# Optimization experiments

Hardware: AMD Instinct MI355X
Metric: run time of the kernel (lower is better)

Reference implementation:

```python
import jax, jax.numpy as jnp
import numpy as np

D_MODEL = 1024
NUM_HEADS = 16
HEAD_DIM = D_MODEL // NUM_HEADS
WINDOW = 64
BATCH = 2
SEQ = 2048


def setup_inputs() -> dict:
    key = jax.random.key(0)
    ks = jax.random.split(key, 5)
    s = 1.0 / np.sqrt(D_MODEL)  # torch Linear-ish init scale
    x = jax.random.normal(ks[0], (BATCH, SEQ, D_MODEL), dtype=jnp.float32)
    Wq = jax.random.normal(ks[1], (D_MODEL, D_MODEL), dtype=jnp.float32) * s
    Wk = jax.random.normal(ks[2], (D_MODEL, D_MODEL), dtype=jnp.float32) * s
    Wv = jax.random.normal(ks[3], (D_MODEL, D_MODEL), dtype=jnp.float32) * s
    Wo = jax.random.normal(ks[4], (D_MODEL, D_MODEL), dtype=jnp.float32) * s
    z = jnp.zeros((D_MODEL,), dtype=jnp.float32)
    return {"x": x, "Wq": Wq, "bq": z, "Wk": Wk, "bk": z, "Wv": Wv, "bv": z,
            "Wo": Wo, "bo": z}


def reference(x, Wq, bq, Wk, bk, Wv, bv, Wo, bo):
    B, S, D = x.shape
    H, Hd = NUM_HEADS, HEAD_DIM
    # QKV projections; weights stored as [in, out] so y = x @ W + b
    q = (x @ Wq + bq).reshape(B, S, H, Hd).transpose(0, 2, 1, 3)  # bhsd
    k = (x @ Wk + bk).reshape(B, S, H, Hd).transpose(0, 2, 1, 3)
    v = (x @ Wv + bv).reshape(B, S, H, Hd).transpose(0, 2, 1, 3)
    scores = jnp.einsum('bhqd,bhkd->bhqk', q, k) / jnp.sqrt(jnp.float32(Hd))
    # static local-window band mask: attend only where |i - j| <= window_size
    idx = jnp.arange(S)
    dist = jnp.abs(idx[None, :] - idx[:, None])  # [S, S]
    scores = jnp.where(dist[None, None] > WINDOW, -jnp.inf, scores)
    attn = jax.nn.softmax(scores, axis=-1)
    out = jnp.einsum('bhqk,bhkd->bhqd', attn, v)
    out = out.transpose(0, 2, 1, 3).reshape(B, S, D)
    return out @ Wo + bo
```

## Files before the change

kernel.cpp:

```cpp
#include <hip/hip_runtime.h>
#include <cstdint>
#include <cstddef>

typedef __bf16 bf16x8 __attribute__((ext_vector_type(8)));
typedef float  f32x4  __attribute__((ext_vector_type(4)));

__device__ __forceinline__ unsigned short f2bf(float f) {
    union { __bf16 b; unsigned short u; } cv; cv.b = (__bf16)f; return cv.u;
}
__device__ __forceinline__ int iclamp(int v, int lo, int hi) {
    return v < lo ? lo : (v > hi ? hi : v);
}

__device__ __forceinline__ void gload16(const void* gsrc, void* ldsdst) {
    __builtin_amdgcn_global_load_lds(
        (const __attribute__((address_space(1))) unsigned int*)(uintptr_t)gsrc,
        (__attribute__((address_space(3))) unsigned int*)(uintptr_t)ldsdst,
        16, 0, 0);
}

#define MFMA16(a, b, c) __builtin_amdgcn_mfma_f32_16x16x32_bf16((a), (b), (c), 0, 0, 0)

__global__ __launch_bounds__(256) void prep_k(const float* __restrict__ x,
                                              const float* __restrict__ Wq,
                                              const float* __restrict__ Wk,
                                              const float* __restrict__ Wv,
                                              const float* __restrict__ Wo,
                                              const float* __restrict__ bq,
                                              const float* __restrict__ bk,
                                              const float* __restrict__ bv,
                                              unsigned short* __restrict__ xb,
                                              unsigned short* __restrict__ Wt,
                                              float* __restrict__ bc) {
    __shared__ float tile[64][65];
    const int bx = blockIdx.x, tid = threadIdx.x;
    if (bx < 1024) {
        const int z = bx >> 8, t = bx & 255;
        const float* W = (z == 0) ? Wq : (z == 1) ? Wk : (z == 2) ? Wv : Wo;
        const int n0 = (t & 15) * 64, k0 = (t >> 4) * 64;
        const int tr = tid >> 4, tc = (tid & 15) * 4;
#pragma unroll
        for (int i = 0; i < 4; ++i) {
            int r = tr + i * 16;
            float4 v = *(const float4*)(W + (size_t)(k0 + r) * 1024 + n0 + tc);
            tile[r][tc + 0] = v.x; tile[r][tc + 1] = v.y;
            tile[r][tc + 2] = v.z; tile[r][tc + 3] = v.w;
        }
        __syncthreads();
        const int n = tid & 63, kc = (tid >> 6) * 16;
        union { unsigned short u[16]; uint4 q[2]; } pk;
#pragma unroll
        for (int c = 0; c < 16; ++c) pk.u[c] = f2bf(tile[kc + c][n]);
        uint4* dst = (uint4*)(Wt + (size_t)z * 1048576 + (size_t)(n0 + n) * 1024 + k0 + kc);
        dst[0] = pk.q[0]; dst[1] = pk.q[1];
    } else if (bx < 3072) {
        size_t i = ((size_t)(bx - 1024) * 256 + tid) * 8;
        float4 a = *(const float4*)(x + i);
        float4 b = *(const float4*)(x + i + 4);
        union { unsigned short u[8]; uint4 q; } pk;
        pk.u[0] = f2bf(a.x); pk.u[1] = f2bf(a.y); pk.u[2] = f2bf(a.z); pk.u[3] = f2bf(a.w);
        pk.u[4] = f2bf(b.x); pk.u[5] = f2bf(b.y); pk.u[6] = f2bf(b.z); pk.u[7] = f2bf(b.w);
        *(uint4*)(xb + i) = pk.q;
    } else {
        int i = (bx - 3072) * 256 + tid;
        bc[i] = (i < 1024) ? bq[i] : (i < 2048) ? bk[i - 1024] : bv[i - 2048];
    }
}

__global__ __launch_bounds__(256, 3) void gemm_qkv(const unsigned short* __restrict__ xb,
                                                   const unsigned short* __restrict__ Wt,
                                                   const float* __restrict__ bcat,
                                                   unsigned short* __restrict__ Qb,
                                                   unsigned short* __restrict__ Kb,
                                                   unsigned short* __restrict__ Vt) {
    __shared__ __align__(16) unsigned short Asm[128 * 64];
    __shared__ __align__(16) unsigned short Bsm[128 * 64];
    const int tid = threadIdx.x, wave = tid >> 6, lane = tid & 63;
    const int lq = lane & 15, quad = lane >> 4;
    const int m0 = blockIdx.y * 128, n0 = blockIdx.x * 128;

    f32x4 acc[4][4];
#pragma unroll
    for (int i = 0; i < 4; ++i)
#pragma unroll
        for (int j = 0; j < 4; ++j) acc[i][j] = f32x4{0.f, 0.f, 0.f, 0.f};

    const int nloc = (wave & 1) * 64;
    float bi[4];
#pragma unroll
    for (int j = 0; j < 4; ++j) bi[j] = bcat[n0 + nloc + j * 16 + lq];

    const int r8 = lane >> 3, cs = lane & 7;
    const int gch = (cs ^ r8) * 8;
    const unsigned short* gA[4];
    const unsigned short* gB[4];
    unsigned short* lA[4];
    unsigned short* lB[4];
#pragma unroll
    for (int s = 0; s < 4; ++s) {
        const int r = wave * 32 + s * 8 + r8;
        gA[s] = xb + (size_t)(m0 + r) * 1024 + gch;
        gB[s] = Wt + (size_t)(n0 + r) * 1024 + gch;
        lA[s] = Asm + (wave * 32 + s * 8) * 64;
        lB[s] = Bsm + (wave * 32 + s * 8) * 64;
    }

    int offA[4][2], offB[4][2];
#pragma unroll
    for (int i = 0; i < 4; ++i)
#pragma unroll
        for (int kk = 0; kk < 2; ++kk) {
            const int rA = (wave >> 1) * 64 + i * 16 + lq;
            const int rB = (wave & 1) * 64 + i * 16 + lq;
            offA[i][kk] = rA * 64 + (((kk * 4 + quad) ^ (lq & 7)) * 8);
            offB[i][kk] = rB * 64 + (((kk * 4 + quad) ^ (lq & 7)) * 8);
        }

    for (int kt = 0; kt < 1024; kt += 64) {
#pragma unroll
        for (int s = 0; s < 4; ++s) gload16(gA[s] + kt, lA[s]);
#pragma unroll
        for (int s = 0; s < 4; ++s) gload16(gB[s] + kt, lB[s]);
        __syncthreads();
#pragma unroll
        for (int kk = 0; kk < 2; ++kk) {
            bf16x8 af[4], bfr[4];
#pragma unroll
            for (int i = 0; i < 4; ++i) af[i] = *(const bf16x8*)(Asm + offA[i][kk]);
#pragma unroll
            for (int j = 0; j < 4; ++j) bfr[j] = *(const bf16x8*)(Bsm + offB[j][kk]);
#pragma unroll
            for (int i = 0; i < 4; ++i)
#pragma unroll
                for (int j = 0; j < 4; ++j)
                    acc[i][j] = MFMA16(af[i], bfr[j], acc[i][j]);
        }
        __syncthreads();
    }

    const int p = n0 >> 10;
    const int c64 = (n0 + nloc) & 1023;
    const int h = c64 >> 6;
    const int b = m0 >> 11;
    const int mw = m0 + (wave >> 1) * 64;
    const int mloc = mw & 2047;
    unsigned short* sw = Asm + wave * 1152;

    unsigned short* qkbase = (p == 0) ? Qb : Kb;

#pragma unroll
    for (int i = 0; i < 4; ++i) {
#pragma unroll
        for (int j = 0; j < 4; ++j)
#pragma unroll
            for (int r = 0; r < 4; ++r)
                sw[(quad * 4 + r) * 72 + j * 16 + lq] = f2bf(acc[i][j][r] + bi[j]);
        if (p < 2) {
            const int row = lane >> 2, c0 = (lane & 3) * 8;
            uint4 v0 = *(const uint4*)(sw + row * 72 + c0);
            uint4 v1 = *(const uint4*)(sw + row * 72 + c0 + 32);
            const int s = mloc + i * 16 + row;
            unsigned short* dp = qkbase + ((size_t)((b * 16 + h) * 2048 + s)) * 64;
            *(uint4*)(dp + c0) = v0;
            *(uint4*)(dp + c0 + 32) = v1;
        } else {
#pragma unroll
            for (int th = 0; th < 2; ++th) {
                union { unsigned short u[8]; uint4 q; } pk;
#pragma unroll
                for (int t = 0; t < 8; ++t) pk.u[t] = sw[(th * 8 + t) * 72 + lane];
                const int sbase = mloc + i * 16 + th * 8;
                *(uint4*)(Vt + ((size_t)((b * 16 + h) * 64 + lane)) * 2048 + sbase) = pk.q;
            }
        }
    }
}

__global__ __launch_bounds__(256, 4) void attn_k(const unsigned short* __restrict__ Qb,
                                                 const unsigned short* __restrict__ Kb,
                                                 const unsigned short* __restrict__ Vt,
                                                 unsigned short* __restrict__ AO) {
    __shared__ __align__(16) unsigned short P[4][16 * 168];
    const int tid = threadIdx.x, wave = tid >> 6, lane = tid & 63;
    const int lq = lane & 15, quad = lane >> 4;
    const int b = blockIdx.z, h = blockIdx.y;
    const int q0 = blockIdx.x * 64 + wave * 16;
    const bool edge = (blockIdx.x == 0) || (blockIdx.x == 31);
    const unsigned short* Qh = Qb + (size_t)((b * 16 + h) * 2048) * 64;
    const unsigned short* Kh = Kb + (size_t)((b * 16 + h) * 2048) * 64;
    const unsigned short* Vh = Vt + (size_t)((b * 16 + h) * 64) * 2048;
    unsigned short* pw = P[wave];

    {
        unsigned int* zp = (unsigned int*)(pw + (lane >> 2) * 168 + 144 + (lane & 3) * 4);
        zp[0] = 0u; zp[1] = 0u;
    }

    const bf16x8 qa0 = *(const bf16x8*)(Qh + (size_t)(q0 + lq) * 64 + quad * 8);
    const bf16x8 qa1 = *(const bf16x8*)(Qh + (size_t)(q0 + lq) * 64 + 32 + quad * 8);

    float pr[9][4];
    float ls[4] = {0.f, 0.f, 0.f, 0.f};
#pragma unroll
    for (int t = 0; t < 9; ++t) {
        const int krow = q0 - 64 + t * 16 + lq;
        const bool need_mask = (t == 0) || (t == 8) || edge;
        const int krc = need_mask ? iclamp(krow, 0, 2047) : krow;
        const unsigned short* kp = Kh + (size_t)krc * 64 + quad * 8;
        const bf16x8 kf0 = *(const bf16x8*)kp;
        const bf16x8 kf1 = *(const bf16x8*)(kp + 32);
        f32x4 cacc = f32x4{0.f, 0.f, 0.f, 0.f};
        cacc = MFMA16(qa0, kf0, cacc);
        cacc = MFMA16(qa1, kf1, cacc);
        if (need_mask) {
#pragma unroll
            for (int r = 0; r < 4; ++r) {
                const int q = q0 + quad * 4 + r;
                const int dj = q - krow;
                const bool ok = (krow >= 0) && (krow < 2048) && (dj <= 64) && (dj >= -64);
                const float pv = ok ? __expf(cacc[r] * 0.125f) : 0.f;
                pr[t][r] = pv;
                ls[r] += pv;
            }
        } else {
#pragma unroll
            for (int r = 0; r < 4; ++r) {
                const float pv = __expf(cacc[r] * 0.125f);
                pr[t][r] = pv;
                ls[r] += pv;
            }
        }
    }
#pragma unroll
    for (int r = 0; r < 4; ++r) {
#pragma unroll
        for (int off = 1; off < 16; off <<= 1)
            ls[r] += __shfl_xor(ls[r], off);
    }
    float rinv[4];
#pragma unroll
    for (int r = 0; r < 4; ++r) rinv[r] = 1.f / ls[r];

#pragma unroll
    for (int t = 0; t < 9; ++t)
#pragma unroll
        for (int r = 0; r < 4; ++r)
            pw[(quad * 4 + r) * 168 + t * 16 + lq] = f2bf(pr[t][r]);

    f32x4 oa[4];
#pragma unroll
    for (int dt = 0; dt < 4; ++dt) oa[dt] = f32x4{0.f, 0.f, 0.f, 0.f};
#pragma unroll
    for (int ks = 0; ks < 5; ++ks) {
        const bf16x8 pf = *(const bf16x8*)(pw + lq * 168 + ks * 32 + quad * 8);
        int s0 = q0 - 64 + ks * 32 + quad * 8;
        s0 = iclamp(s0, 0, 2040);
#pragma unroll
        for (int dt = 0; dt < 4; ++dt) {
            const bf16x8 vf = *(const bf16x8*)(Vh + (size_t)(dt * 16 + lq) * 2048 + s0);
            oa[dt] = MFMA16(pf, vf, oa[dt]);
        }
    }

#pragma unroll
    for (int dt = 0; dt < 4; ++dt)
#pragma unroll
        for (int r = 0; r < 4; ++r)
            pw[(quad * 4 + r) * 72 + dt * 16 + lq] = f2bf(oa[dt][r] * rinv[r]);
    {
        const int row = lane >> 2, c0 = (lane & 3) * 16;
        uint4 v0 = *(const uint4*)(pw + row * 72 + c0);
        uint4 v1 = *(const uint4*)(pw + row * 72 + c0 + 8);
        unsigned short* dp = AO + (size_t)(b * 2048 + q0 + row) * 1024 + h * 64 + c0;
        *(uint4*)(dp) = v0;
        *(uint4*)(dp + 8) = v1;
    }
}

__global__ __launch_bounds__(256, 2) void gemm_out(const unsigned short* __restrict__ AO,
                                                   const unsigned short* __restrict__ Wot,
                                                   const float* __restrict__ bo,
                                                   float* __restrict__ out) {
    __shared__ __align__(16) unsigned short Asm[128 * 64];
    __shared__ __align__(16) unsigned short Bsm[64 * 64];
    const int tid = threadIdx.x, wave = tid >> 6, lane = tid & 63;
    const int lq = lane & 15, quad = lane >> 4;
    const int m0 = blockIdx.y * 128, n0 = blockIdx.x * 64;

    f32x4 acc[4][2];
#pragma unroll
    for (int i = 0; i < 4; ++i)
#pragma unroll
        for (int j = 0; j < 2; ++j) acc[i][j] = f32x4{0.f, 0.f, 0.f, 0.f};

    float bi[2];
#pragma unroll
    for (int j = 0; j < 2; ++j) bi[j] = bo[n0 + (wave & 1) * 32 + j * 16 + lq];

    const int r8 = lane >> 3, cs = lane & 7;
    const int gch = (cs ^ r8) * 8;
    const unsigned short* gA[4];
    unsigned short* lA[4];
#pragma unroll
    for (int s = 0; s < 4; ++s) {
        const int r = wave * 32 + s * 8 + r8;
        gA[s] = AO + (size_t)(m0 + r) * 1024 + gch;
        lA[s] = Asm + (wave * 32 + s * 8) * 64;
    }
    const unsigned short* gB[2];
    unsigned short* lB[2];
#pragma unroll
    for (int s = 0; s < 2; ++s) {
        const int r = wave * 16 + s * 8 + r8;
        gB[s] = Wot + (size_t)(n0 + r) * 1024 + gch;
        lB[s] = Bsm + (wave * 16 + s * 8) * 64;
    }

    int offA[4][2], offB[2][2];
#pragma unroll
    for (int kk = 0; kk < 2; ++kk) {
#pragma unroll
        for (int i = 0; i < 4; ++i) {
            const int rA = (wave >> 1) * 64 + i * 16 + lq;
            offA[i][kk] = rA * 64 + (((kk * 4 + quad) ^ (lq & 7)) * 8);
        }
#pragma unroll
        for (int j = 0; j < 2; ++j) {
            const int rB = (wave & 1) * 32 + j * 16 + lq;
            offB[j][kk] = rB * 64 + (((kk * 4 + quad) ^ (lq & 7)) * 8);
        }
    }

    for (int kt = 0; kt < 1024; kt += 64) {
#pragma unroll
        for (int s = 0; s < 4; ++s) gload16(gA[s] + kt, lA[s]);
#pragma unroll
        for (int s = 0; s < 2; ++s) gload16(gB[s] + kt, lB[s]);
        __syncthreads();
#pragma unroll
        for (int kk = 0; kk < 2; ++kk) {
            bf16x8 af[4], bfr[2];
#pragma unroll
            for (int i = 0; i < 4; ++i) af[i] = *(const bf16x8*)(Asm + offA[i][kk]);
#pragma unroll
            for (int j = 0; j < 2; ++j) bfr[j] = *(const bf16x8*)(Bsm + offB[j][kk]);
#pragma unroll
            for (int i = 0; i < 4; ++i)
#pragma unroll
                for (int j = 0; j < 2; ++j)
                    acc[i][j] = MFMA16(af[i], bfr[j], acc[i][j]);
        }
        __syncthreads();
    }

    float* swf = (float*)Asm + wave * 528;
    const int row = lane >> 2, c0 = (lane & 3) * 8;
    const size_t obase = (size_t)(m0 + (wave >> 1) * 64) * 1024 + n0 + (wave & 1) * 32;
#pragma unroll
    for (int i = 0; i < 4; ++i) {
#pragma unroll
        for (int j = 0; j < 2; ++j)
#pragma unroll
            for (int r = 0; r < 4; ++r)
                swf[(quad * 4 + r) * 33 + j * 16 + lq] = acc[i][j][r] + bi[j];
        float4 v0, v1;
        v0.x = swf[row * 33 + c0 + 0]; v0.y = swf[row * 33 + c0 + 1];
        v0.z = swf[row * 33 + c0 + 2]; v0.w = swf[row * 33 + c0 + 3];
        v1.x = swf[row * 33 + c0 + 4]; v1.y = swf[row * 33 + c0 + 5];
        v1.z = swf[row * 33 + c0 + 6]; v1.w = swf[row * 33 + c0 + 7];
        float* op = out + obase + (size_t)(i * 16 + row) * 1024 + c0;
        *(float4*)(op) = v0;
        *(float4*)(op + 4) = v1;
    }
}

extern "C" void kernel_launch(void* const* d_in, const int* in_sizes, int n_in,
                              void* d_out, int out_size, void* d_ws, size_t ws_size,
                              hipStream_t stream) {
    const float* x  = (const float*)d_in[0];
    const float* Wq = (const float*)d_in[1];
    const float* bq = (const float*)d_in[2];
    const float* Wk = (const float*)d_in[3];
    const float* bk = (const float*)d_in[4];
    const float* Wv = (const float*)d_in[5];
    const float* bv = (const float*)d_in[6];
    const float* Wo = (const float*)d_in[7];
    const float* bo = (const float*)d_in[8];
    float* out = (float*)d_out;

    unsigned short* us = (unsigned short*)d_ws;
    const size_t MEG = 1048576;
    unsigned short* xb = us;
    unsigned short* Wt = us + 4 * MEG;
    unsigned short* Qb = us + 8 * MEG;
    unsigned short* Kb = us + 12 * MEG;
    unsigned short* Vt = us + 16 * MEG;
    unsigned short* AO = us + 20 * MEG;
    float* bcat = (float*)(us + 24 * MEG);

    prep_k<<<3084, 256, 0, stream>>>(x, Wq, Wk, Wv, Wo, bq, bk, bv, xb, Wt, bcat);
    gemm_qkv<<<dim3(24, 32), 256, 0, stream>>>(xb, Wt, bcat, Qb, Kb, Vt);
    attn_k<<<dim3(32, 16, 2), 256, 0, stream>>>(Qb, Kb, Vt, AO);
    gemm_out<<<dim3(16, 32), 256, 0, stream>>>(AO, Wt + 3 * MEG, bo, out);
}
```

Measured before the change: 163.4 us.

## Rewrite QKV GEMM with 256x192 tiles, double-buffered LDS and phased MFMA scheduling

The QKV projection GEMM moves from 128x128 tiles with 4 waves and a single LDS buffer to 256x192 tiles with 8 waves. Global-to-LDS loads for the next-but-one k-tile are issued while MFMAs run on the current one, using explicit vmcnt waits, barriers, sched_barrier and setprio. The aim is to hide global load latency and raise operand reuse per block. The cost is more LDS use, tighter register pressure from 24 accumulators per wave, and a fragile hand-written synchronisation schedule. The epilogue is reworked to scatter 48-column slices into Q, K and the transposed V.

New measurement: 161.2 us. No clear change (-1.4%).

```diff
diff --git a/kernel.cpp b/kernel.cpp
--- a/kernel.cpp
+++ b/kernel.cpp
@@ -67,110 +67,155 @@
     }
 }
 
-__global__ __launch_bounds__(256, 3) void gemm_qkv(const unsigned short* __restrict__ xb,
+
+#define QKV_BAR   __builtin_amdgcn_s_barrier()
+#define QKV_SB0   __builtin_amdgcn_sched_barrier(0)
+#define QKV_LGKM0 asm volatile("s_waitcnt lgkmcnt(0)" ::: "memory")
+#define QKV_VM7   asm volatile("s_waitcnt vmcnt(7)" ::: "memory")
+#define QKV_VM0   asm volatile("s_waitcnt vmcnt(0)" ::: "memory")
+#define QKV_PRIO1 __builtin_amdgcn_s_setprio(1)
+#define QKV_PRIO0 __builtin_amdgcn_s_setprio(0)
+
+#define PHASE_READS(AB, I0)                                                    \
+    af00 = *(const bf16x8*)((AB) + aRow + (I0) * 1024 + sw0);                  \
+    af01 = *(const bf16x8*)((AB) + aRow + (I0) * 1024 + sw1);                  \
+    af10 = *(const bf16x8*)((AB) + aRow + (I0) * 1024 + 1024 + sw0);           \
+    af11 = *(const bf16x8*)((AB) + aRow + (I0) * 1024 + 1024 + sw1);
+
+#define PHASE_MFMA(I0)                                                         \
+    acc[(I0)][0]     = MFMA16(af00, b00, acc[(I0)][0]);                        \
+    acc[(I0)][0]     = MFMA16(af01, b10, acc[(I0)][0]);                        \
+    acc[(I0)][1]     = MFMA16(af00, b01, acc[(I0)][1]);                        \
+    acc[(I0)][1]     = MFMA16(af01, b11, acc[(I0)][1]);                        \
+    acc[(I0)][2]     = MFMA16(af00, b02, acc[(I0)][2]);                        \
+    acc[(I0)][2]     = MFMA16(af01, b12, acc[(I0)][2]);                        \
+    acc[(I0) + 1][0] = MFMA16(af10, b00, acc[(I0) + 1][0]);                    \
+    acc[(I0) + 1][0] = MFMA16(af11, b10, acc[(I0) + 1][0]);                    \
+    acc[(I0) + 1][1] = MFMA16(af10, b01, acc[(I0) + 1][1]);                    \
+    acc[(I0) + 1][1] = MFMA16(af11, b11, acc[(I0) + 1][1]);                    \
+    acc[(I0) + 1][2] = MFMA16(af10, b02, acc[(I0) + 1][2]);                    \
+    acc[(I0) + 1][2] = MFMA16(af11, b12, acc[(I0) + 1][2]);
+
+#define STAGE_T(BOA, BOB, KT) do {                                             \
+    gload16(gA0 + (KT), lA0 + (BOA)); gload16(gA1 + (KT), lA1 + (BOA));        \
+    gload16(gA2 + (KT), lA2 + (BOA)); gload16(gA3 + (KT), lA3 + (BOA));        \
+    gload16(gB0 + (KT), lB0 + (BOB)); gload16(gB1 + (KT), lB1 + (BOB));        \
+    gload16(gB2 + (KT), lB2 + (BOB)); } while (0)
+
+#define KTILE(AB, BB, BOA, BOB, T) do {                                        \
+    bf16x8 af00, af01, af10, af11;                                             \
+    bf16x8 b00, b10, b01, b11, b02, b12;                                       \
+    b00 = *(const bf16x8*)((BB) + bRow + sw0);                                 \
+    b10 = *(const bf16x8*)((BB) + bRow + sw1);                                 \
+    b01 = *(const bf16x8*)((BB) + bRow + 1024 + sw0);                          \
+    b11 = *(const bf16x8*)((BB) + bRow + 1024 + sw1);                          \
+    b02 = *(const bf16x8*)((BB) + bRow + 2048 + sw0);                          \
+    b12 = *(const bf16x8*)((BB) + bRow + 2048 + sw1);                          \
+    PHASE_READS(AB, 0);                                                        \
+    QKV_BAR; QKV_LGKM0; QKV_SB0;                                               \
+    QKV_PRIO1; PHASE_MFMA(0); QKV_PRIO0; QKV_BAR;                              \
+    PHASE_READS(AB, 2);                                                        \
+    QKV_BAR; QKV_LGKM0; QKV_SB0;                                               \
+    QKV_PRIO1; PHASE_MFMA(2); QKV_PRIO0; QKV_BAR;                              \
+    PHASE_READS(AB, 4);                                                        \
+    QKV_BAR; QKV_LGKM0; QKV_SB0;                                               \
+    QKV_PRIO1; PHASE_MFMA(4); QKV_PRIO0; QKV_BAR;                              \
+    PHASE_READS(AB, 6);                                                        \
+    QKV_LGKM0; QKV_SB0; QKV_BAR;                                               \
+    if ((T) < 14) STAGE_T((BOA), (BOB), (T) * 64 + 128);                       \
+    QKV_PRIO1; PHASE_MFMA(6); QKV_PRIO0;                                       \
+    if ((T) < 14)      { QKV_VM7; QKV_SB0; QKV_BAR; }                          \
+    else if ((T) < 15) { QKV_VM0; QKV_SB0; QKV_BAR; }                          \
+} while (0)
+
+__global__ __launch_bounds__(512, 2) void gemm_qkv(const unsigned short* __restrict__ xb,
                                                    const unsigned short* __restrict__ Wt,
                                                    const float* __restrict__ bcat,
                                                    unsigned short* __restrict__ Qb,
                                                    unsigned short* __restrict__ Kb,
                                                    unsigned short* __restrict__ Vt) {
-    __shared__ __align__(16) unsigned short Asm[128 * 64];
-    __shared__ __align__(16) unsigned short Bsm[128 * 64];
+    __shared__ __align__(16) unsigned short Asm[2 * 256 * 64];
+    __shared__ __align__(16) unsigned short Bsm[2 * 192 * 64];
     const int tid = threadIdx.x, wave = tid >> 6, lane = tid & 63;
     const int lq = lane & 15, quad = lane >> 4;
-    const int m0 = blockIdx.y * 128, n0 = blockIdx.x * 128;
-
-    f32x4 acc[4][4];
-#pragma unroll
-    for (int i = 0; i < 4; ++i)
-#pragma unroll
-        for (int j = 0; j < 4; ++j) acc[i][j] = f32x4{0.f, 0.f, 0.f, 0.f};
-
-    const int nloc = (wave & 1) * 64;
-    float bi[4];
-#pragma unroll
-    for (int j = 0; j < 4; ++j) bi[j] = bcat[n0 + nloc + j * 16 + lq];
+    const int wr = wave >> 2, wc = wave & 3;
+    const int m0 = blockIdx.x * 256, n0 = blockIdx.y * 192;
+
+    f32x4 acc[8][3];
+#pragma unroll
+    for (int i = 0; i < 8; ++i)
+#pragma unroll
+        for (int j = 0; j < 3; ++j) acc[i][j] = f32x4{0.f, 0.f, 0.f, 0.f};
+
+    float bi[3];
+#pragma unroll
+    for (int j = 0; j < 3; ++j) bi[j] = bcat[n0 + wc * 48 + j * 16 + lq];
 
     const int r8 = lane >> 3, cs = lane & 7;
     const int gch = (cs ^ r8) * 8;
-    const unsigned short* gA[4];
-    const unsigned short* gB[4];
-    unsigned short* lA[4];
-    unsigned short* lB[4];
-#pragma unroll
-    for (int s = 0; s < 4; ++s) {
-        const int r = wave * 32 + s * 8 + r8;
-        gA[s] = xb + (size_t)(m0 + r) * 1024 + gch;
-        gB[s] = Wt + (size_t)(n0 + r) * 1024 + gch;
-        lA[s] = Asm + (wave * 32 + s * 8) * 64;
-        lB[s] = Bsm + (wave * 32 + s * 8) * 64;
-    }
-
-    int offA[4][2], offB[4][2];
-#pragma unroll
-    for (int i = 0; i < 4; ++i)
-#pragma unroll
-        for (int kk = 0; kk < 2; ++kk) {
-            const int rA = (wave >> 1) * 64 + i * 16 + lq;
-            const int rB = (wave & 1) * 64 + i * 16 + lq;
-            offA[i][kk] = rA * 64 + (((kk * 4 + quad) ^ (lq & 7)) * 8);
-            offB[i][kk] = rB * 64 + (((kk * 4 + quad) ^ (lq & 7)) * 8);
-        }
-
-    for (int kt = 0; kt < 1024; kt += 64) {
-#pragma unroll
-        for (int s = 0; s < 4; ++s) gload16(gA[s] + kt, lA[s]);
-#pragma unroll
-        for (int s = 0; s < 4; ++s) gload16(gB[s] + kt, lB[s]);
-        __syncthreads();
-#pragma unroll
-        for (int kk = 0; kk < 2; ++kk) {
-            bf16x8 af[4], bfr[4];
-#pragma unroll
-            for (int i = 0; i < 4; ++i) af[i] = *(const bf16x8*)(Asm + offA[i][kk]);
-#pragma unroll
-            for (int j = 0; j < 4; ++j) bfr[j] = *(const bf16x8*)(Bsm + offB[j][kk]);
-#pragma unroll
-            for (int i = 0; i < 4; ++i)
-#pragma unroll
-                for (int j = 0; j < 4; ++j)
-                    acc[i][j] = MFMA16(af[i], bfr[j], acc[i][j]);
-        }
-        __syncthreads();
-    }
-
-    const int p = n0 >> 10;
-    const int c64 = (n0 + nloc) & 1023;
-    const int h = c64 >> 6;
+    const unsigned short* gA0 = xb + (size_t)(m0 +   0 + wave * 8 + r8) * 1024 + gch;
+    const unsigned short* gA1 = xb + (size_t)(m0 +  64 + wave * 8 + r8) * 1024 + gch;
+    const unsigned short* gA2 = xb + (size_t)(m0 + 128 + wave * 8 + r8) * 1024 + gch;
+    const unsigned short* gA3 = xb + (size_t)(m0 + 192 + wave * 8 + r8) * 1024 + gch;
+    const unsigned short* gB0 = Wt + (size_t)(n0 +   0 + wave * 8 + r8) * 1024 + gch;
+    const unsigned short* gB1 = Wt + (size_t)(n0 +  64 + wave * 8 + r8) * 1024 + gch;
+    const unsigned short* gB2 = Wt + (size_t)(n0 + 128 + wave * 8 + r8) * 1024 + gch;
+    unsigned short* lA0 = Asm + (  0 + wave * 8) * 64;
+    unsigned short* lA1 = Asm + ( 64 + wave * 8) * 64;
+    unsigned short* lA2 = Asm + (128 + wave * 8) * 64;
+    unsigned short* lA3 = Asm + (192 + wave * 8) * 64;
+    unsigned short* lB0 = Bsm + (  0 + wave * 8) * 64;
+    unsigned short* lB1 = Bsm + ( 64 + wave * 8) * 64;
+    unsigned short* lB2 = Bsm + (128 + wave * 8) * 64;
+
+    const int sw0 = ((quad)     ^ (lq & 7)) * 8;
+    const int sw1 = ((4 + quad) ^ (lq & 7)) * 8;
+    const int aRow = (wr * 128 + lq) * 64;
+    const int bRow = (wc * 48  + lq) * 64;
+
+    STAGE_T(0, 0, 0);
+    STAGE_T(16384, 12288, 64);
+    QKV_VM7; QKV_SB0; QKV_BAR;
+
+    for (int u = 0; u < 8; ++u) {
+        const int t0 = u * 2;
+        KTILE(Asm,          Bsm,          0,     0,     t0);
+        KTILE(Asm + 16384,  Bsm + 12288,  16384, 12288, t0 + 1);
+    }
+
     const int b = m0 >> 11;
-    const int mw = m0 + (wave >> 1) * 64;
-    const int mloc = mw & 2047;
-    unsigned short* sw = Asm + wave * 1152;
-
-    unsigned short* qkbase = (p == 0) ? Qb : Kb;
-
-#pragma unroll
-    for (int i = 0; i < 4; ++i) {
-#pragma unroll
-        for (int j = 0; j < 4; ++j)
+    const int mb = (m0 & 2047) + wr * 128;
+    unsigned short* sw = Asm + wave * 1024;
+    const int row32 = lane >> 1, half = lane & 1;
+#pragma unroll
+    for (int i = 0; i < 8; ++i) {
+#pragma unroll
+        for (int j = 0; j < 3; ++j)
 #pragma unroll
             for (int r = 0; r < 4; ++r)
-                sw[(quad * 4 + r) * 72 + j * 16 + lq] = f2bf(acc[i][j][r] + bi[j]);
-        if (p < 2) {
-            const int row = lane >> 2, c0 = (lane & 3) * 8;
-            uint4 v0 = *(const uint4*)(sw + row * 72 + c0);
-            uint4 v1 = *(const uint4*)(sw + row * 72 + c0 + 32);
-            const int s = mloc + i * 16 + row;
-            unsigned short* dp = qkbase + ((size_t)((b * 16 + h) * 2048 + s)) * 64;
-            *(uint4*)(dp + c0) = v0;
-            *(uint4*)(dp + c0 + 32) = v1;
-        } else {
-#pragma unroll
-            for (int th = 0; th < 2; ++th) {
-                union { unsigned short u[8]; uint4 q; } pk;
-#pragma unroll
-                for (int t = 0; t < 8; ++t) pk.u[t] = sw[(th * 8 + t) * 72 + lane];
-                const int sbase = mloc + i * 16 + th * 8;
-                *(uint4*)(Vt + ((size_t)((b * 16 + h) * 64 + lane)) * 2048 + sbase) = pk.q;
+                sw[(quad * 4 + r) * 56 + j * 16 + lq] = f2bf(acc[i][j][r] + bi[j]);
+        const int sb = mb + i * 16;
+#pragma unroll
+        for (int j = 0; j < 3; ++j) {
+            const int c0 = n0 + wc * 48 + j * 16;
+            const int p = c0 >> 10, ch = c0 & 1023;
+            const int h = ch >> 6, d0 = ch & 63;
+            if (p < 2) {
+                unsigned short* base = (p == 0) ? Qb : Kb;
+                if (lane < 32) {
+                    uint4 v = *(const uint4*)(sw + row32 * 56 + j * 16 + half * 8);
+                    *(uint4*)(base + ((size_t)((b * 16 + h) * 2048 + sb + row32)) * 64
+                              + d0 + half * 8) = v;
+                }
+            } else {
+                if (lane < 32) {
+                    union { unsigned short u[8]; uint4 q; } pk;
+#pragma unroll
+                    for (int q2 = 0; q2 < 8; ++q2)
+                        pk.u[q2] = sw[(half * 8 + q2) * 56 + j * 16 + row32];
+                    *(uint4*)(Vt + ((size_t)((b * 16 + h) * 64 + d0 + row32)) * 2048
+                              + sb + half * 8) = pk.q;
+                }
             }
         }
     }
@@ -399,7 +444,7 @@
     float* bcat = (float*)(us + 24 * MEG);
 
     prep_k<<<3084, 256, 0, stream>>>(x, Wq, Wk, Wv, Wo, bq, bk, bv, xb, Wt, bcat);
-    gemm_qkv<<<dim3(24, 32), 256, 0, stream>>>(xb, Wt, bcat, Qb, Kb, Vt);
+    gemm_qkv<<<dim3(16, 16), 512, 0, stream>>>(xb, Wt, bcat, Qb, Kb, Vt);
     attn_k<<<dim3(32, 16, 2), 256, 0, stream>>>(Qb, Kb, Vt, AO);
     gemm_out<<<dim3(16, 32), 256, 0, stream>>>(AO, Wt + 3 * MEG, bo, out);
 }
```
